# Kernel optimization log

Hardware: AMD Instinct MI355X
Metric: run time of the kernel (lower is better)

Reference implementation:

```python
import jax, jax.numpy as jnp
import numpy as np

B = 4096
HIST = 50
VOCAB = 100000
PAD_IDX = 179
EMB_DIM = 64           # sparse_dim_after_embedding
DENSE = 256            # dense_feature_number
PROJ_IN = 768          # emb_feature_dim_before_project
PROJ_HID = 256
PROJ_OUT = 64          # emb_feature_dim
BOT = (512, 64)        # bottom_mlp_dims
ALL_DIM = EMB_DIM + BOT[1] + PROJ_OUT        # 192
OUT_DIM = ALL_DIM * (ALL_DIM + 1) // 2 + BOT[1]  # 18592
TOP = (1024, 512)      # top_mlp_dims
BN_EPS = 1e-5

# precomputed upper-triangular (incl. diagonal) indices, row-major like torch mask extract
_TRIU_R, _TRIU_C = np.triu_indices(ALL_DIM)


def setup_inputs() -> dict:
    key = jax.random.key(0)
    ks = jax.random.split(key, 20)
    s = 0.02
    emb_table = jax.random.normal(ks[0], (VOCAB, EMB_DIM), jnp.float32) * s
    emb_table = emb_table.at[PAD_IDX].set(0.0)  # padding_idx=179
    return {
        "x_sparse": jax.random.randint(ks[1], (B, HIST), 0, VOCAB),
        "x_dense": jax.random.normal(ks[2], (B, DENSE), jnp.float32),
        "x_embed_before_projection": jax.random.normal(ks[3], (B, PROJ_IN), jnp.float32),
        "emb_table": emb_table,
        "pw1": jax.random.normal(ks[4], (PROJ_IN, PROJ_HID), jnp.float32) * s,
        "pb1": jnp.zeros((PROJ_HID,), jnp.float32),
        "pw2": jax.random.normal(ks[5], (PROJ_HID, PROJ_OUT), jnp.float32) * s,
        "pb2": jnp.zeros((PROJ_OUT,), jnp.float32),
        "bn_gamma": jnp.ones((PROJ_OUT,), jnp.float32),
        "bn_beta": jnp.zeros((PROJ_OUT,), jnp.float32),
        "bw1": jax.random.normal(ks[6], (DENSE, BOT[0]), jnp.float32) * s,
        "bb1": jnp.zeros((BOT[0],), jnp.float32),
        "bw2": jax.random.normal(ks[7], (BOT[0], BOT[1]), jnp.float32) * s,
        "bb2": jnp.zeros((BOT[1],), jnp.float32),
        "tw1": jax.random.normal(ks[8], (OUT_DIM, TOP[0]), jnp.float32) * s,
        "tb1": jnp.zeros((TOP[0],), jnp.float32),
        "tw2": jax.random.normal(ks[9], (TOP[0], TOP[1]), jnp.float32) * s,
        "tb2": jnp.zeros((TOP[1],), jnp.float32),
        "tw3": jax.random.normal(ks[10], (TOP[1], 1), jnp.float32) * s,
        "tb3": jnp.zeros((1,), jnp.float32),
    }


def reference(x_sparse, x_dense, x_embed_before_projection, emb_table,
              pw1, pb1, pw2, pb2, bn_gamma, bn_beta,
              bw1, bb1, bw2, bb2, tw1, tb1, tw2, tb2, tw3, tb3):
    # embedding-sum over history: [B, HIST, EMB_DIM] -> [B, EMB_DIM]
    embed_x = jnp.sum(emb_table[x_sparse], axis=1)

    # ContrastiveNet: Linear -> ReLU -> Linear -> BatchNorm1d (batch stats, training fwd)
    h = jax.nn.relu(x_embed_before_projection @ pw1 + pb1)
    z = h @ pw2 + pb2
    mu = jnp.mean(z, axis=0)
    var = jnp.var(z, axis=0)  # biased variance, as torch BN uses for normalization
    x_embed = bn_gamma * (z - mu) * jax.lax.rsqrt(var + BN_EPS) + bn_beta

    # bottom MLP (dropout = identity at inference)
    bottom = jax.nn.relu(jax.nn.relu(x_dense @ bw1 + bb1) @ bw2 + bb2)

    concat_first = jnp.concatenate([bottom, x_embed, embed_x], axis=-1)  # [B, 192]

    # pairwise dot-product interaction; pack upper triangle incl. diagonal
    dot = jnp.einsum('bi,bj->bij', concat_first, concat_first)  # [B, 192, 192]
    interaction = dot[:, _TRIU_R, _TRIU_C]  # [B, 192*193/2]

    concat_second = jnp.concatenate([interaction, bottom], axis=-1)  # [B, OUT_DIM]

    t = jax.nn.relu(concat_second @ tw1 + tb1)
    t = jax.nn.relu(t @ tw2 + tb2)
    output = jax.nn.sigmoid(t @ tw3 + tb3)  # [B, 1]
    # squeeze(-1).squeeze().unsqueeze(1) -> [B, 1]
    output = output.reshape(-1, 1)
    return output, x_embed
```

## Files before the change

### kernel.cpp

```cpp
#include <hip/hip_runtime.h>
#include <hip/hip_bf16.h>
#include <cstdint>
#include <cstddef>

typedef __bf16 bf16;
typedef unsigned char u8;
typedef unsigned short u16;
typedef __bf16 v8bf  __attribute__((ext_vector_type(8)));
typedef float  f32x4 __attribute__((ext_vector_type(4)));
typedef float  f32x16 __attribute__((ext_vector_type(16)));
typedef int    i32x4 __attribute__((ext_vector_type(4)));
typedef int    v8i32 __attribute__((ext_vector_type(8)));

__device__ __forceinline__ void async16(void* lds, const void* g) {
  __builtin_amdgcn_global_load_lds(
      (const __attribute__((address_space(1))) unsigned int*)g,
      (__attribute__((address_space(3))) unsigned int*)lds, 16, 0, 0);
}


__device__ __forceinline__ void pairs_dev(u16* __restrict__ pairs) {
  int r = threadIdx.x;
  if (r < 192) {
    int off = 192 * r - (r * (r - 1)) / 2;
    for (int c = r; c < 192; ++c) pairs[off + c - r] = (u16)((r << 8) | c);
  } else if (r == 192) {
    for (int j = 0; j < 64; ++j) pairs[18528 + j] = (u16)((j << 8) | 192);
  } else if (r == 193) {
    for (int j = 18592; j < 18624; ++j) pairs[j] = (u16)((192 << 8) | 192);
  }
}

__device__ __forceinline__ void packA_dev(const float* __restrict__ A,
                                          bf16* __restrict__ Ap, int K,
                                          int bx, int by) {
  const int t = threadIdx.x;
  const int KT = K >> 5;
  const size_t tile = ((size_t)bx * KT + by) * (64 * 32);
  const int c = t;
  const int mm = c >> 2, koct = (c & 3) * 8;
  const float* src = A + (size_t)(bx * 64 + mm) * K + by * 32 + koct;
  f32x4 f0 = *(const f32x4*)src;
  f32x4 f1 = *(const f32x4*)(src + 4);
  __align__(16) bf16 h[8];
  h[0]=(bf16)f0[0]; h[1]=(bf16)f0[1]; h[2]=(bf16)f0[2]; h[3]=(bf16)f0[3];
  h[4]=(bf16)f1[0]; h[5]=(bf16)f1[1]; h[6]=(bf16)f1[2]; h[7]=(bf16)f1[3];
  *(i32x4*)(Ap + tile + (size_t)c * 8) = *(const i32x4*)h;
}

__device__ __forceinline__ void packB_dev(const float* __restrict__ B,
                                          bf16* __restrict__ Bp, int K, int N,
                                          int bx, int by,
                                          float* __restrict__ sLB) {
  const int BNp = 64, LS = 66;
  const int t = threadIdx.x;
  const int KT = K >> 5;
  for (int idx = t; idx < 32 * BNp; idx += 256) {
    const int kk = idx >> 6, nn = idx & 63;
    sLB[kk * LS + nn] = B[(size_t)(by * 32 + kk) * N + bx * BNp + nn];
  }
  __syncthreads();
  const size_t tile = ((size_t)bx * KT + by) * ((size_t)BNp * 32);
  for (int c = t; c < BNp * 4; c += 256) {
    const int nn = c >> 2, koct = (c & 3) * 8;
    __align__(16) bf16 h[8];
#pragma unroll
    for (int j = 0; j < 8; ++j) h[j] = (bf16)sLB[(koct + j) * LS + nn];
    *(i32x4*)(Bp + tile + (size_t)c * 8) = *(const i32x4*)h;
  }
}

__device__ __forceinline__ void packTw1_dev(const float* __restrict__ tw1,
                                            u8* __restrict__ Bp, int nt, int kw,
                                            float* __restrict__ sLB) {
  const int t = threadIdx.x;
  u8* tile = Bp + ((size_t)nt * 291 + kw) * 8192;
#pragma unroll
  for (int ph = 0; ph < 2; ++ph) {
    if (ph) __syncthreads();
#pragma unroll
    for (int idx = t; idx < 1024; idx += 256) {
      const int kk = idx >> 5, nn4 = (idx & 31) * 4;
      const int gk = kw * 64 + ph * 32 + kk;
      f32x4 v = f32x4{0.f, 0.f, 0.f, 0.f};
      if (gk < 18592) {
        v = *(const f32x4*)(tw1 + (size_t)gk * 1024 + nt * 128 + nn4);
        v *= 32.f;
      }
      *(f32x4*)(sLB + kk * 132 + nn4) = v;
    }
    __syncthreads();
    const int nn = t >> 1;
    const int hkb = (t & 1) * 16;
    const int c = nn * 4 + ph * 2 + (t & 1);
    i32x4 d;
#pragma unroll
    for (int g = 0; g < 4; ++g) {
      const float p0 = sLB[(hkb + g * 4 + 0) * 132 + nn];
      const float p1 = sLB[(hkb + g * 4 + 1) * 132 + nn];
      const float p2 = sLB[(hkb + g * 4 + 2) * 132 + nn];
      const float p3 = sLB[(hkb + g * 4 + 3) * 132 + nn];
      int r = __builtin_amdgcn_cvt_pk_fp8_f32(p0, p1, 0, false);
      r = __builtin_amdgcn_cvt_pk_fp8_f32(p2, p3, r, true);
      d[g] = r;
    }
    *(i32x4*)(tile + c * 16) = d;
  }
}

__global__ __launch_bounds__(256) void prologue_kernel(
    const float* __restrict__ xep, const float* __restrict__ xd,
    const float* __restrict__ pw1, const float* __restrict__ pw2,
    const float* __restrict__ bw1, const float* __restrict__ bw2,
    const float* __restrict__ tw1, const float* __restrict__ tw2,
    bf16* Xp, bf16* Xd, bf16* Bpw1, bf16* Bpw2, bf16* Bbw1, bf16* Bbw2,
    u8* Btw1, bf16* Btw2, u16* pairs) {
  __shared__ float sLB[32 * 132];
  int i = blockIdx.x;
  if (i < 2328) { packTw1_dev(tw1, Btw1, i & 7, i >> 3, sLB); return; }
  i -= 2328;
  if (i < 1536) { packA_dev(xep, Xp, 768, i & 63, i >> 6); return; }
  i -= 1536;
  if (i < 512)  { packA_dev(xd, Xd, 256, i & 63, i >> 6); return; }
  i -= 512;
  if (i < 96)   { packB_dev(pw1, Bpw1, 768, 256, i & 3, i >> 2, sLB); return; }
  i -= 96;
  if (i < 8)    { packB_dev(pw2, Bpw2, 256, 64, 0, i, sLB); return; }
  i -= 8;
  if (i < 64)   { packB_dev(bw1, Bbw1, 256, 512, i & 7, i >> 3, sLB); return; }
  i -= 64;
  if (i < 16)   { packB_dev(bw2, Bbw2, 512, 64, 0, i, sLB); return; }
  i -= 16;
  if (i < 256)  { packB_dev(tw2, Btw2, 1024, 512, i & 7, i >> 3, sLB); return; }
  i -= 256;
  if (i == 0) pairs_dev(pairs);
}

__device__ __forceinline__ void embed8_dev(const int* __restrict__ xs,
                                           const float* __restrict__ emb,
                                           float* __restrict__ cf, int blk) {
  const int wid = threadIdx.x >> 6, lane = threadIdx.x & 63;
#pragma unroll
  for (int s = 0; s < 2; ++s) {
    const int b = blk * 8 + s * 4 + wid;
    const int* row = xs + (size_t)b * 50;
    float acc = 0.f;
#pragma unroll 10
    for (int h = 0; h < 50; ++h) {
      int idx = row[h];
      acc += emb[(size_t)idx * 64 + lane];
    }
    cf[(size_t)b * 193 + 128 + lane] = acc;
  }
}

template <int BM, int BN, int MF, int NF>
__device__ __forceinline__ void gemm_body(
    const bf16* __restrict__ Ap, const bf16* __restrict__ Bp,
    const float* __restrict__ bias,
    float* __restrict__ outF, int ldF,
    bf16* __restrict__ outP, int ktN, int bmsh,
    int KT, int M0, int relu_flag, int bx, int by,
    bf16* sA, bf16* sB) {
  const int t = threadIdx.x;
  const int wid = t >> 6, lane = t & 63;
  const int wm = (wid >> 1) * (MF * 16);
  const int wn = (wid & 1) * (NF * 16);
  const int r16 = lane & 15, q = lane >> 4;

  f32x4 acc[MF][NF];
#pragma unroll
  for (int i = 0; i < MF; ++i)
#pragma unroll
    for (int j = 0; j < NF; ++j) acc[i][j] = f32x4{0.f, 0.f, 0.f, 0.f};

  const bf16* aBase = Ap + (size_t)bx * KT * (BM * 32);
  const bf16* bBase = Bp + (size_t)by * KT * (BN * 32);
  constexpr int A_CH = BM * 4;
  constexpr int B_CH = BN * 4;

  for (int kt = 0; kt < KT; ++kt) {
    const bf16* ag = aBase + (size_t)kt * (BM * 32);
    const bf16* bg = bBase + (size_t)kt * (BN * 32);
#pragma unroll
    for (int c = t; c < A_CH; c += 256) {
      const int row = c >> 2, qs = c & 3, qg = (qs - (row >> 1)) & 3;
      async16(sA + c * 8, ag + row * 32 + qg * 8);
    }
#pragma unroll
    for (int c = t; c < B_CH; c += 256) {
      const int row = c >> 2, qs = c & 3, qg = (qs - (row >> 1)) & 3;
      async16(sB + c * 8, bg + row * 32 + qg * 8);
    }
    __syncthreads();
    v8bf af[MF], bfr[NF];
#pragma unroll
    for (int i = 0; i < MF; ++i) {
      const int row = wm + i * 16 + r16;
      af[i] = *(const v8bf*)(sA + row * 32 + (((q + (row >> 1)) & 3) * 8));
    }
#pragma unroll
    for (int j = 0; j < NF; ++j) {
      const int row = wn + j * 16 + r16;
      bfr[j] = *(const v8bf*)(sB + row * 32 + (((q + (row >> 1)) & 3) * 8));
    }
#pragma unroll
    for (int i = 0; i < MF; ++i)
#pragma unroll
      for (int j = 0; j < NF; ++j)
        acc[i][j] = __builtin_amdgcn_mfma_f32_16x16x32_bf16(af[i], bfr[j], acc[i][j], 0, 0, 0);
    __syncthreads();
  }

#pragma unroll
  for (int j = 0; j < NF; ++j) {
    const int gn = by * BN + wn + j * 16 + r16;
    const float bv = bias[gn];
#pragma unroll
    for (int i = 0; i < MF; ++i) {
      const int gm0 = M0 + bx * BM + wm + i * 16 + q * 4;
#pragma unroll
      for (int r = 0; r < 4; ++r) {
        float v = acc[i][j][r] + bv;
        if (relu_flag) v = fmaxf(v, 0.f);
        const int gm = gm0 + r;
        if (outF) outF[(size_t)gm * ldF + gn] = v;
        if (outP) {
          const int mt = gm >> bmsh, mm = gm & ((1 << bmsh) - 1);
          outP[(((size_t)mt * ktN + (gn >> 5)) << (bmsh + 5)) + ((size_t)mm << 5) + (gn & 31)] = (bf16)v;
        }
      }
    }
  }
}

template <int BM, int BN, int MF, int NF>
__global__ __launch_bounds__(256, 2) void gemm_kernel(
    const bf16* __restrict__ Ap, const bf16* __restrict__ Bp,
    const float* __restrict__ bias,
    float* __restrict__ outF, int ldF,
    bf16* __restrict__ outP, int ktN, int bmsh,
    int KT, int M0, int relu_flag) {
  __shared__ __align__(16) bf16 sA[BM * 32];
  __shared__ __align__(16) bf16 sB[BN * 32];
  gemm_body<BM, BN, MF, NF>(Ap, Bp, bias, outF, ldF, outP, ktN, bmsh,
                            KT, M0, relu_flag, blockIdx.x, blockIdx.y, sA, sB);
}

template <int BM, int BN, int MF, int NF>
__global__ __launch_bounds__(256, 2) void gemm_dual_kernel(
    const bf16* Ap0, const bf16* Bp0, const float* bias0,
    float* outF0, int ldF0, bf16* outP0, int ktN0, int bmsh0, int KT0, int relu0, int gy0,
    const bf16* Ap1, const bf16* Bp1, const float* bias1,
    float* outF1, int ldF1, bf16* outP1, int ktN1, int bmsh1, int KT1, int relu1, int gy1,
    const int* xs, const float* emb, float* cf) {
  __shared__ __align__(16) bf16 sA[BM * 32];
  __shared__ __align__(16) bf16 sB[BN * 32];
  if (blockIdx.z == 0) {
    if ((int)blockIdx.y >= gy0) return;
    gemm_body<BM, BN, MF, NF>(Ap0, Bp0, bias0, outF0, ldF0, outP0, ktN0, bmsh0,
                              KT0, 0, relu0, blockIdx.x, blockIdx.y, sA, sB);
  } else if (blockIdx.z == 1) {
    if ((int)blockIdx.y >= gy1) return;
    gemm_body<BM, BN, MF, NF>(Ap1, Bp1, bias1, outF1, ldF1, outP1, ktN1, bmsh1,
                              KT1, 0, relu1, blockIdx.x, blockIdx.y, sA, sB);
  } else {
    embed8_dev(xs, emb, cf, blockIdx.y * 64 + blockIdx.x);
  }
}

template <int S>
__global__ __launch_bounds__(256, 4) void gemm_splitk_mx(
    const u8* __restrict__ Ap, const u8* __restrict__ Bp,
    bf16* __restrict__ part, int Mchunk) {
  __shared__ __align__(16) u8 sAB[4][8192];
  const int t = threadIdx.x;
  const int bx = blockIdx.x, by = blockIdx.y, bz = blockIdx.z;
  const int lane = t & 63, wid = t >> 6;
  const int wm = (wid >> 1) * 64, wn = (wid & 1) * 64;
  const int l31 = lane & 31, khalf = lane >> 5;
  const int kw0 = (291 * bz) / S, kw1 = (291 * (bz + 1)) / S;

  const int r1 = t >> 2;
  const int g1 = r1 * 64 + ((((t & 3) - (r1 >> 1)) & 3) << 4);
  const int r2 = (t + 256) >> 2;
  const int g2 = r2 * 64 + (((((t + 256) & 3) - (r2 >> 1)) & 3) << 4);
  u8* lA = &sAB[0][0] + t * 16;
  u8* lB = &sAB[2][0] + t * 16;

  const u8* fa0[2]; const u8* fa1[2]; const u8* fb0[2]; const u8* fb1[2];
#pragma unroll
  for (int i = 0; i < 2; ++i) {
    const int ra = wm + i * 32 + l31;
    const int qa = (khalf * 2 + (ra >> 1)) & 3;
    fa0[i] = &sAB[0][0] + ra * 64 + qa * 16;
    fa1[i] = &sAB[0][0] + ra * 64 + (((qa + 1) & 3) << 4);
    const int rb = wn + i * 32 + l31;
    const int qb = (khalf * 2 + (rb >> 1)) & 3;
    fb0[i] = &sAB[2][0] + rb * 64 + qb * 16;
    fb1[i] = &sAB[2][0] + rb * 64 + (((qb + 1) & 3) << 4);
  }

  f32x16 acc[2][2];
#pragma unroll
  for (int i = 0; i < 2; ++i)
#pragma unroll
    for (int j = 0; j < 2; ++j)
#pragma unroll
      for (int r = 0; r < 16; ++r) acc[i][j][r] = 0.f;

  const u8* agp = Ap + ((size_t)bx * 291 + kw0) * 8192;
  const u8* bgp = Bp + ((size_t)by * 291 + kw0) * 8192;

  auto compute = [&](int off) {
    v8i32 av[2], bv[2];
#pragma unroll
    for (int i = 0; i < 2; ++i) {
      union { i32x4 h[2]; v8i32 v; } ua;
      ua.h[0] = *(const i32x4*)(fa0[i] + off);
      ua.h[1] = *(const i32x4*)(fa1[i] + off);
      av[i] = ua.v;
      union { i32x4 h[2]; v8i32 v; } ub;
      ub.h[0] = *(const i32x4*)(fb0[i] + off);
      ub.h[1] = *(const i32x4*)(fb1[i] + off);
      bv[i] = ub.v;
    }
#pragma unroll
    for (int i = 0; i < 2; ++i)
#pragma unroll
      for (int j = 0; j < 2; ++j)
        acc[i][j] = __builtin_amdgcn_mfma_scale_f32_32x32x64_f8f6f4(
            av[i], bv[j], acc[i][j], 0, 0,
            0, 0x7F7F7F7F,
            0, 0x7A7A7A7A);
  };

  const int nw = kw1 - kw0;
  int w = 0;
  for (; w + 2 <= nw; w += 2) {
    async16(lA, agp + g1);         async16(lA + 4096, agp + g2);
    async16(lB, bgp + g1);         async16(lB + 4096, bgp + g2);
    async16(lA + 8192, agp + 8192 + g1); async16(lA + 12288, agp + 8192 + g2);
    async16(lB + 8192, bgp + 8192 + g1); async16(lB + 12288, bgp + 8192 + g2);
    agp += 16384; bgp += 16384;
    __syncthreads();
    compute(0);
    compute(8192);
    __syncthreads();
  }
  if (w < nw) {
    async16(lA, agp + g1); async16(lA + 4096, agp + g2);
    async16(lB, bgp + g1); async16(lB + 4096, bgp + g2);
    __syncthreads();
    compute(0);
    __syncthreads();
  }

  bf16* pBase = part + (size_t)bz * Mchunk * 1024;
#pragma unroll
  for (int i = 0; i < 2; ++i)
#pragma unroll
    for (int j = 0; j < 2; ++j) {
      const int gn = by * 128 + wn + j * 32 + l31;
#pragma unroll
      for (int r = 0; r < 16; ++r) {
        const int gm = bx * 128 + wm + i * 32 + (r & 3) + 8 * (r >> 2) + 4 * khalf;
        pBase[(size_t)gm * 1024 + gn] = (bf16)acc[i][j][r];
      }
    }
}

__global__ __launch_bounds__(256) void reducek_kernel(const bf16* __restrict__ part,
                                                      const float* __restrict__ bias,
                                                      bf16* __restrict__ t1,
                                                      int S, int Mchunk, int M0) {
  const int idx = blockIdx.x * 256 + threadIdx.x;
  const int gm = idx >> 7;
  const int gn8 = (idx & 127) * 8;
  float v[8] = {0.f, 0.f, 0.f, 0.f, 0.f, 0.f, 0.f, 0.f};
  for (int s = 0; s < S; ++s) {
    v8bf p = *(const v8bf*)(part + ((size_t)s * Mchunk + gm) * 1024 + gn8);
#pragma unroll
    for (int r = 0; r < 8; ++r) v[r] += (float)p[r];
  }
  const f32x4 b0 = *(const f32x4*)(bias + gn8);
  const f32x4 b1 = *(const f32x4*)(bias + gn8 + 4);
  __align__(16) bf16 h[8];
#pragma unroll
  for (int r = 0; r < 4; ++r) h[r] = (bf16)fmaxf(v[r] + b0[r], 0.f);
#pragma unroll
  for (int r = 0; r < 4; ++r) h[4 + r] = (bf16)fmaxf(v[4 + r] + b1[r], 0.f);
  const int G = M0 + gm;
  const int mt = G >> 6, mm = G & 63, kt = gn8 >> 5;
  *(i32x4*)(t1 + (((size_t)mt * 32 + kt) << 11) + (mm << 5) + (gn8 & 31)) = *(const i32x4*)h;
}

__global__ __launch_bounds__(256) void bnstats_kernel(const float* __restrict__ z,
                                                      float* __restrict__ stats) {
  const int j = blockIdx.x, t = threadIdx.x;
  float s = 0.f, s2 = 0.f;
  for (int b = t; b < 4096; b += 256) {
    float v = z[(size_t)b * 64 + j];
    s += v; s2 += v * v;
  }
  __shared__ float sh[256], sh2[256];
  sh[t] = s; sh2[t] = s2;
  __syncthreads();
  for (int o = 128; o > 0; o >>= 1) {
    if (t < o) { sh[t] += sh[t + o]; sh2[t] += sh2[t + o]; }
    __syncthreads();
  }
  if (t == 0) {
    float mu = sh[0] * (1.f / 4096.f);
    float var = sh2[0] * (1.f / 4096.f) - mu * mu;
    stats[j] = mu;
    stats[64 + j] = rsqrtf(var + 1e-5f);
  }
}

__global__ __launch_bounds__(256, 2) void agen_kernel(const float* __restrict__ cf,
                                                      const float* __restrict__ z,
                                                      const float* __restrict__ stats,
                                                      const float* __restrict__ gamma,
                                                      const float* __restrict__ beta,
                                                      const u16* __restrict__ pairs,
                                                      u8* __restrict__ Ap,
                                                      float* __restrict__ dout,
                                                      int rowBase) {
  __shared__ float sCF[64 * 193];
  const int t = threadIdx.x;
  const int gRow0 = rowBase + blockIdx.x * 64;
  for (int idx = t; idx < 64 * 64; idx += 256) {
    const int r = idx >> 6, c = idx & 63;
    sCF[r * 193 + c] = cf[(size_t)(gRow0 + r) * 193 + c];
  }
  for (int idx = t; idx < 64 * 64; idx += 256) {
    const int r = idx >> 6, c = idx & 63;
    sCF[r * 193 + 128 + c] = cf[(size_t)(gRow0 + r) * 193 + 128 + c];
  }
  for (int idx = t; idx < 64 * 64; idx += 256) {
    const int r = idx >> 6, c = idx & 63;
    const float xe = gamma[c] * (z[(size_t)(gRow0 + r) * 64 + c] - stats[c]) * stats[64 + c] + beta[c];
    sCF[r * 193 + 64 + c] = xe;
    if (blockIdx.y == 0) dout[4096 + (size_t)(gRow0 + r) * 64 + c] = xe;
  }
  if (t < 64) sCF[t * 193 + 192] = 1.f;
  __syncthreads();

  const int kw0 = (291 * blockIdx.y) / 8;
  const int kw1 = (291 * (blockIdx.y + 1)) / 8;
  const int row = t >> 2, kq = t & 3;
  const int mt = blockIdx.x >> 1;
  const int mrow = (blockIdx.x & 1) * 64 + row;
  const float* myrow = sCF + row * 193;
  for (int kw = kw0; kw < kw1; ++kw) {
    const int kb = kw * 64 + kq * 16;
    i32x4 d;
    if (kb >= 18592) {
      d = i32x4{0, 0, 0, 0};
    } else {
      union { i32x4 v4[2]; u16 u[16]; } P;
      P.v4[0] = *(const i32x4*)(pairs + kb);
      P.v4[1] = *(const i32x4*)(pairs + kb + 8);
#pragma unroll
      for (int g = 0; g < 4; ++g) {
        float p[4];
#pragma unroll
        for (int j = 0; j < 4; ++j) {
          const u16 pr = P.u[g * 4 + j];
          p[j] = myrow[pr >> 8] * myrow[pr & 255];
        }
        int r = __builtin_amdgcn_cvt_pk_fp8_f32(p[0], p[1], 0, false);
        r = __builtin_amdgcn_cvt_pk_fp8_f32(p[2], p[3], r, true);
        d[g] = r;
      }
    }
    *(i32x4*)(Ap + (((size_t)mt * 291 + kw) * 128 + mrow) * 64 + kq * 16) = d;
  }
}

__global__ __launch_bounds__(256) void topdot_kernel(const float* __restrict__ t2,
                                                     const float* __restrict__ w,
                                                     const float* __restrict__ b3,
                                                     float* __restrict__ dout) {
  const int wid = threadIdx.x >> 6, lane = threadIdx.x & 63;
  const int b = blockIdx.x * 4 + wid;
  const f32x4* row = (const f32x4*)(t2 + (size_t)b * 512);
  const f32x4* wv = (const f32x4*)w;
  float s = 0.f;
#pragma unroll
  for (int i = 0; i < 2; ++i) {
    f32x4 a = row[lane * 2 + i], c = wv[lane * 2 + i];
    s += a[0] * c[0] + a[1] * c[1] + a[2] * c[2] + a[3] * c[3];
  }
  for (int m = 32; m > 0; m >>= 1) s += __shfl_xor(s, m, 64);
  if (lane == 0) dout[b] = 1.f / (1.f + __expf(-(s + b3[0])));
}

extern "C" void kernel_launch(void* const* d_in, const int* in_sizes, int n_in,
                              void* d_out, int out_size, void* d_ws, size_t ws_size,
                              hipStream_t stream) {
  const int*   xs   = (const int*)  d_in[0];
  const float* xd   = (const float*)d_in[1];
  const float* xep  = (const float*)d_in[2];
  const float* emb  = (const float*)d_in[3];
  const float* pw1  = (const float*)d_in[4];
  const float* pb1  = (const float*)d_in[5];
  const float* pw2  = (const float*)d_in[6];
  const float* pb2  = (const float*)d_in[7];
  const float* gmma = (const float*)d_in[8];
  const float* beta = (const float*)d_in[9];
  const float* bw1  = (const float*)d_in[10];
  const float* bb1  = (const float*)d_in[11];
  const float* bw2  = (const float*)d_in[12];
  const float* bb2  = (const float*)d_in[13];
  const float* tw1  = (const float*)d_in[14];
  const float* tb1  = (const float*)d_in[15];
  const float* tw2  = (const float*)d_in[16];
  const float* tb2  = (const float*)d_in[17];
  const float* tw3  = (const float*)d_in[18];
  const float* tb3  = (const float*)d_in[19];
  float* out = (float*)d_out;

  uint8_t* base = (uint8_t*)d_ws;
  size_t off = 0;
  auto alloc = [&](size_t b) {
    void* p = base + off;
    off = (off + b + 511) & ~((size_t)511);
    return p;
  };
  u16*  pairs = (u16*) alloc((size_t)18624 * 2);
  bf16* Xp    = (bf16*)alloc((size_t)4096 * 768 * 2);
  bf16* Xd    = (bf16*)alloc((size_t)4096 * 256 * 2);
  bf16* Bpw1  = (bf16*)alloc((size_t)768 * 256 * 2);
  bf16* Bpw2  = (bf16*)alloc((size_t)256 * 64 * 2);
  bf16* Bbw1  = (bf16*)alloc((size_t)256 * 512 * 2);
  bf16* Bbw2  = (bf16*)alloc((size_t)512 * 64 * 2);
  u8*   Btw1  = (u8*)  alloc((size_t)8 * 291 * 8192);
  bf16* Btw2  = (bf16*)alloc((size_t)1024 * 512 * 2);
  bf16* hbuf  = (bf16*)alloc((size_t)4096 * 256 * 2);
  float* z    = (float*)alloc((size_t)4096 * 64 * 4);
  float* stats= (float*)alloc((size_t)128 * 4);
  bf16* b0    = (bf16*)alloc((size_t)4096 * 512 * 2);
  float* cf   = (float*)alloc((size_t)4096 * 193 * 4);
  bf16* t1    = (bf16*)alloc((size_t)4096 * 1024 * 2);
  float* t2   = (float*)alloc((size_t)4096 * 512 * 4);
  size_t fixedEnd = off;

  int chunk = 512, S = 8;
  {
    const int candC[5] = {4096, 2048, 2048, 1024, 512};
    const int candS[5] = {4, 8, 4, 8, 8};
    for (int i = 0; i < 5; ++i) {
      size_t need = fixedEnd + (size_t)candC[i] * 18624 + 1024 +
                    (size_t)candS[i] * candC[i] * 1024 * 2 + 1024;
      if (need <= ws_size) { chunk = candC[i]; S = candS[i]; break; }
    }
  }
  u8*   ApBig = (u8*)  alloc((size_t)chunk * 18624);
  bf16* partK = (bf16*)alloc((size_t)S * chunk * 1024 * 2);

  prologue_kernel<<<4817, 256, 0, stream>>>(
      xep, xd, pw1, pw2, bw1, bw2, tw1, tw2,
      Xp, Xd, Bpw1, Bpw2, Bbw1, Bbw2, Btw1, Btw2, pairs);

  gemm_dual_kernel<64, 64, 2, 2><<<dim3(64, 8, 3), 256, 0, stream>>>(
      Xp, Bpw1, pb1, nullptr, 0, hbuf, 8, 6, 24, 1, 4,
      Xd, Bbw1, bb1, nullptr, 0, b0, 16, 6, 8, 1, 8,
      xs, emb, cf);
  gemm_dual_kernel<64, 64, 2, 2><<<dim3(64, 1, 2), 256, 0, stream>>>(
      hbuf, Bpw2, pb2, z, 64, nullptr, 0, 0, 8, 0, 1,
      b0, Bbw2, bb2, cf, 193, nullptr, 0, 0, 16, 1, 1,
      nullptr, nullptr, nullptr);

  bnstats_kernel<<<64, 256, 0, stream>>>(z, stats);

  for (int c0 = 0; c0 < 4096; c0 += chunk) {
    agen_kernel<<<dim3(chunk / 64, 8), 256, 0, stream>>>(
        cf, z, stats, gmma, beta, pairs, ApBig, out, c0);
    if (S == 4)
      gemm_splitk_mx<4><<<dim3(chunk / 128, 8, 4), 256, 0, stream>>>(
          ApBig, Btw1, partK, chunk);
    else
      gemm_splitk_mx<8><<<dim3(chunk / 128, 8, 8), 256, 0, stream>>>(
          ApBig, Btw1, partK, chunk);
    reducek_kernel<<<chunk / 2, 256, 0, stream>>>(partK, tb1, t1, S, chunk, c0);
  }

  gemm_kernel<64, 64, 2, 2><<<dim3(64, 8), 256, 0, stream>>>(
      t1, Btw2, tb2, t2, 512, nullptr, 0, 0, 32, 0, 1);
  topdot_kernel<<<1024, 256, 0, stream>>>(t2, tw3, tb3, out);
}
```

Baseline: 353.6 us.

## Fuse BN stats into GEMM epilogue, simplify tw1 packing, store t2 as bf16

Removes the separate batch-norm statistics kernel by accumulating column sums and sums of squares with atomics in the z GEMM epilogue, with the stats buffer zeroed in the prologue. The tw1 FP8 packing now goes directly from registers to the packed tile instead of staging through shared memory with barriers. The tw2 GEMM writes its output as packed bf16 for the final dot kernel rather than fp32. Risks: the atomic summation order is nondeterministic, the E[x^2]-mu^2 variance is computed from partial sums, and t2 loses precision in bf16.

```diff
diff --git a/kernel.cpp b/kernel.cpp
--- a/kernel.cpp
+++ b/kernel.cpp
@@ -10,6 +10,7 @@
 typedef float  f32x4 __attribute__((ext_vector_type(4)));
 typedef float  f32x16 __attribute__((ext_vector_type(16)));
 typedef int    i32x4 __attribute__((ext_vector_type(4)));
+typedef int    i32x2 __attribute__((ext_vector_type(2)));
 typedef int    v8i32 __attribute__((ext_vector_type(8)));
 
 __device__ __forceinline__ void async16(void* lds, const void* g) {
@@ -19,8 +20,9 @@
 }
 
 
-__device__ __forceinline__ void pairs_dev(u16* __restrict__ pairs) {
+__device__ __forceinline__ void pairs_dev(u16* __restrict__ pairs, float* __restrict__ stats) {
   int r = threadIdx.x;
+  if (r < 128) stats[r] = 0.f;
   if (r < 192) {
     int off = 192 * r - (r * (r - 1)) / 2;
     for (int c = r; c < 192; ++c) pairs[off + c - r] = (u16)((r << 8) | c);
@@ -71,40 +73,31 @@
 }
 
 __device__ __forceinline__ void packTw1_dev(const float* __restrict__ tw1,
-                                            u8* __restrict__ Bp, int nt, int kw,
-                                            float* __restrict__ sLB) {
+                                            u8* __restrict__ Bp, int nt, int kw) {
   const int t = threadIdx.x;
+  const int n4 = t & 31, k8 = t >> 5;
+  const int kbase = kw * 64 + k8 * 8;
+  const int nbase = nt * 128 + n4 * 4;
+  f32x4 v[8];
+#pragma unroll
+  for (int j = 0; j < 8; ++j) {
+    const int gk = kbase + j;
+    if (gk < 18592) {
+      v[j] = *(const f32x4*)(tw1 + (size_t)gk * 1024 + nbase);
+      v[j] *= 32.f;
+    } else {
+      v[j] = f32x4{0.f, 0.f, 0.f, 0.f};
+    }
+  }
   u8* tile = Bp + ((size_t)nt * 291 + kw) * 8192;
 #pragma unroll
-  for (int ph = 0; ph < 2; ++ph) {
-    if (ph) __syncthreads();
-#pragma unroll
-    for (int idx = t; idx < 1024; idx += 256) {
-      const int kk = idx >> 5, nn4 = (idx & 31) * 4;
-      const int gk = kw * 64 + ph * 32 + kk;
-      f32x4 v = f32x4{0.f, 0.f, 0.f, 0.f};
-      if (gk < 18592) {
-        v = *(const f32x4*)(tw1 + (size_t)gk * 1024 + nt * 128 + nn4);
-        v *= 32.f;
-      }
-      *(f32x4*)(sLB + kk * 132 + nn4) = v;
-    }
-    __syncthreads();
-    const int nn = t >> 1;
-    const int hkb = (t & 1) * 16;
-    const int c = nn * 4 + ph * 2 + (t & 1);
-    i32x4 d;
-#pragma unroll
-    for (int g = 0; g < 4; ++g) {
-      const float p0 = sLB[(hkb + g * 4 + 0) * 132 + nn];
-      const float p1 = sLB[(hkb + g * 4 + 1) * 132 + nn];
-      const float p2 = sLB[(hkb + g * 4 + 2) * 132 + nn];
-      const float p3 = sLB[(hkb + g * 4 + 3) * 132 + nn];
-      int r = __builtin_amdgcn_cvt_pk_fp8_f32(p0, p1, 0, false);
-      r = __builtin_amdgcn_cvt_pk_fp8_f32(p2, p3, r, true);
-      d[g] = r;
-    }
-    *(i32x4*)(tile + c * 16) = d;
+  for (int c = 0; c < 4; ++c) {
+    int r0 = __builtin_amdgcn_cvt_pk_fp8_f32(v[0][c], v[1][c], 0, false);
+    r0 = __builtin_amdgcn_cvt_pk_fp8_f32(v[2][c], v[3][c], r0, true);
+    int r1 = __builtin_amdgcn_cvt_pk_fp8_f32(v[4][c], v[5][c], 0, false);
+    r1 = __builtin_amdgcn_cvt_pk_fp8_f32(v[6][c], v[7][c], r1, true);
+    i32x2 d; d[0] = r0; d[1] = r1;
+    *(i32x2*)(tile + (n4 * 4 + c) * 64 + k8 * 8) = d;
   }
 }
 
@@ -114,10 +107,10 @@
     const float* __restrict__ bw1, const float* __restrict__ bw2,
     const float* __restrict__ tw1, const float* __restrict__ tw2,
     bf16* Xp, bf16* Xd, bf16* Bpw1, bf16* Bpw2, bf16* Bbw1, bf16* Bbw2,
-    u8* Btw1, bf16* Btw2, u16* pairs) {
-  __shared__ float sLB[32 * 132];
+    u8* Btw1, bf16* Btw2, u16* pairs, float* stats) {
+  __shared__ float sLB[32 * 66];
   int i = blockIdx.x;
-  if (i < 2328) { packTw1_dev(tw1, Btw1, i & 7, i >> 3, sLB); return; }
+  if (i < 2328) { packTw1_dev(tw1, Btw1, i & 7, i >> 3); return; }
   i -= 2328;
   if (i < 1536) { packA_dev(xep, Xp, 768, i & 63, i >> 6); return; }
   i -= 1536;
@@ -133,7 +126,7 @@
   i -= 16;
   if (i < 256)  { packB_dev(tw2, Btw2, 1024, 512, i & 7, i >> 3, sLB); return; }
   i -= 256;
-  if (i == 0) pairs_dev(pairs);
+  if (i == 0) pairs_dev(pairs, stats);
 }
 
 __device__ __forceinline__ void embed8_dev(const int* __restrict__ xs,
@@ -161,7 +154,7 @@
     float* __restrict__ outF, int ldF,
     bf16* __restrict__ outP, int ktN, int bmsh,
     int KT, int M0, int relu_flag, int bx, int by,
-    bf16* sA, bf16* sB) {
+    bf16* sA, bf16* sB, float* statsAcc) {
   const int t = threadIdx.x;
   const int wid = t >> 6, lane = t & 63;
   const int wm = (wid >> 1) * (MF * 16);
@@ -212,6 +205,10 @@
     __syncthreads();
   }
 
+  float cs[NF], cs2[NF];
+#pragma unroll
+  for (int j = 0; j < NF; ++j) { cs[j] = 0.f; cs2[j] = 0.f; }
+
 #pragma unroll
   for (int j = 0; j < NF; ++j) {
     const int gn = by * BN + wn + j * 16 + r16;
@@ -223,12 +220,27 @@
       for (int r = 0; r < 4; ++r) {
         float v = acc[i][j][r] + bv;
         if (relu_flag) v = fmaxf(v, 0.f);
+        if (statsAcc) { cs[j] += v; cs2[j] += v * v; }
         const int gm = gm0 + r;
         if (outF) outF[(size_t)gm * ldF + gn] = v;
         if (outP) {
           const int mt = gm >> bmsh, mm = gm & ((1 << bmsh) - 1);
           outP[(((size_t)mt * ktN + (gn >> 5)) << (bmsh + 5)) + ((size_t)mm << 5) + (gn & 31)] = (bf16)v;
         }
+      }
+    }
+  }
+
+  if (statsAcc) {
+#pragma unroll
+    for (int j = 0; j < NF; ++j) {
+      float a = cs[j], b2 = cs2[j];
+      a += __shfl_xor(a, 16, 64);  a += __shfl_xor(a, 32, 64);
+      b2 += __shfl_xor(b2, 16, 64); b2 += __shfl_xor(b2, 32, 64);
+      if (q == 0) {
+        const int gn = by * BN + wn + j * 16 + r16;
+        atomicAdd(&statsAcc[gn], a);
+        atomicAdd(&statsAcc[64 + gn], b2);
       }
     }
   }
@@ -244,13 +256,14 @@
   __shared__ __align__(16) bf16 sA[BM * 32];
   __shared__ __align__(16) bf16 sB[BN * 32];
   gemm_body<BM, BN, MF, NF>(Ap, Bp, bias, outF, ldF, outP, ktN, bmsh,
-                            KT, M0, relu_flag, blockIdx.x, blockIdx.y, sA, sB);
+                            KT, M0, relu_flag, blockIdx.x, blockIdx.y, sA, sB, nullptr);
 }
 
 template <int BM, int BN, int MF, int NF>
 __global__ __launch_bounds__(256, 2) void gemm_dual_kernel(
     const bf16* Ap0, const bf16* Bp0, const float* bias0,
     float* outF0, int ldF0, bf16* outP0, int ktN0, int bmsh0, int KT0, int relu0, int gy0,
+    float* statsAcc0,
     const bf16* Ap1, const bf16* Bp1, const float* bias1,
     float* outF1, int ldF1, bf16* outP1, int ktN1, int bmsh1, int KT1, int relu1, int gy1,
     const int* xs, const float* emb, float* cf) {
@@ -259,11 +272,11 @@
   if (blockIdx.z == 0) {
     if ((int)blockIdx.y >= gy0) return;
     gemm_body<BM, BN, MF, NF>(Ap0, Bp0, bias0, outF0, ldF0, outP0, ktN0, bmsh0,
-                              KT0, 0, relu0, blockIdx.x, blockIdx.y, sA, sB);
+                              KT0, 0, relu0, blockIdx.x, blockIdx.y, sA, sB, statsAcc0);
   } else if (blockIdx.z == 1) {
     if ((int)blockIdx.y >= gy1) return;
     gemm_body<BM, BN, MF, NF>(Ap1, Bp1, bias1, outF1, ldF1, outP1, ktN1, bmsh1,
-                              KT1, 0, relu1, blockIdx.x, blockIdx.y, sA, sB);
+                              KT1, 0, relu1, blockIdx.x, blockIdx.y, sA, sB, nullptr);
   } else {
     embed8_dev(xs, emb, cf, blockIdx.y * 64 + blockIdx.x);
   }
@@ -395,32 +408,9 @@
   *(i32x4*)(t1 + (((size_t)mt * 32 + kt) << 11) + (mm << 5) + (gn8 & 31)) = *(const i32x4*)h;
 }
 
-__global__ __launch_bounds__(256) void bnstats_kernel(const float* __restrict__ z,
-                                                      float* __restrict__ stats) {
-  const int j = blockIdx.x, t = threadIdx.x;
-  float s = 0.f, s2 = 0.f;
-  for (int b = t; b < 4096; b += 256) {
-    float v = z[(size_t)b * 64 + j];
-    s += v; s2 += v * v;
-  }
-  __shared__ float sh[256], sh2[256];
-  sh[t] = s; sh2[t] = s2;
-  __syncthreads();
-  for (int o = 128; o > 0; o >>= 1) {
-    if (t < o) { sh[t] += sh[t + o]; sh2[t] += sh2[t + o]; }
-    __syncthreads();
-  }
-  if (t == 0) {
-    float mu = sh[0] * (1.f / 4096.f);
-    float var = sh2[0] * (1.f / 4096.f) - mu * mu;
-    stats[j] = mu;
-    stats[64 + j] = rsqrtf(var + 1e-5f);
-  }
-}
-
 __global__ __launch_bounds__(256, 2) void agen_kernel(const float* __restrict__ cf,
                                                       const float* __restrict__ z,
-                                                      const float* __restrict__ stats,
+                                                      const float* __restrict__ gsum,
                                                       const float* __restrict__ gamma,
                                                       const float* __restrict__ beta,
                                                       const u16* __restrict__ pairs,
@@ -428,6 +418,7 @@
                                                       float* __restrict__ dout,
                                                       int rowBase) {
   __shared__ float sCF[64 * 193];
+  __shared__ float sMu[64], sRstd[64];
   const int t = threadIdx.x;
   const int gRow0 = rowBase + blockIdx.x * 64;
   for (int idx = t; idx < 64 * 64; idx += 256) {
@@ -438,13 +429,20 @@
     const int r = idx >> 6, c = idx & 63;
     sCF[r * 193 + 128 + c] = cf[(size_t)(gRow0 + r) * 193 + 128 + c];
   }
+  if (t < 64) {
+    const float mu = gsum[t] * (1.f / 4096.f);
+    const float var = gsum[64 + t] * (1.f / 4096.f) - mu * mu;
+    sMu[t] = mu;
+    sRstd[t] = rsqrtf(var + 1e-5f);
+    sCF[t * 193 + 192] = 1.f;
+  }
+  __syncthreads();
   for (int idx = t; idx < 64 * 64; idx += 256) {
     const int r = idx >> 6, c = idx & 63;
-    const float xe = gamma[c] * (z[(size_t)(gRow0 + r) * 64 + c] - stats[c]) * stats[64 + c] + beta[c];
+    const float xe = gamma[c] * (z[(size_t)(gRow0 + r) * 64 + c] - sMu[c]) * sRstd[c] + beta[c];
     sCF[r * 193 + 64 + c] = xe;
     if (blockIdx.y == 0) dout[4096 + (size_t)(gRow0 + r) * 64 + c] = xe;
   }
-  if (t < 64) sCF[t * 193 + 192] = 1.f;
   __syncthreads();
 
   const int kw0 = (291 * blockIdx.y) / 8;
@@ -479,20 +477,19 @@
   }
 }
 
-__global__ __launch_bounds__(256) void topdot_kernel(const float* __restrict__ t2,
+__global__ __launch_bounds__(256) void topdot_kernel(const bf16* __restrict__ t2p,
                                                      const float* __restrict__ w,
                                                      const float* __restrict__ b3,
                                                      float* __restrict__ dout) {
   const int wid = threadIdx.x >> 6, lane = threadIdx.x & 63;
   const int b = blockIdx.x * 4 + wid;
-  const f32x4* row = (const f32x4*)(t2 + (size_t)b * 512);
-  const f32x4* wv = (const f32x4*)w;
+  const size_t addr = ((((size_t)(b >> 6) * 16) + (lane >> 2)) << 11) +
+                      ((size_t)(b & 63) << 5) + (lane & 3) * 8;
+  v8bf p = *(const v8bf*)(t2p + addr);
+  const float* wv = w + lane * 8;
   float s = 0.f;
 #pragma unroll
-  for (int i = 0; i < 2; ++i) {
-    f32x4 a = row[lane * 2 + i], c = wv[lane * 2 + i];
-    s += a[0] * c[0] + a[1] * c[1] + a[2] * c[2] + a[3] * c[3];
-  }
+  for (int r = 0; r < 8; ++r) s += (float)p[r] * wv[r];
   for (int m = 32; m > 0; m >>= 1) s += __shfl_xor(s, m, 64);
   if (lane == 0) dout[b] = 1.f / (1.f + __expf(-(s + b3[0])));
 }
@@ -544,7 +541,7 @@
   bf16* b0    = (bf16*)alloc((size_t)4096 * 512 * 2);
   float* cf   = (float*)alloc((size_t)4096 * 193 * 4);
   bf16* t1    = (bf16*)alloc((size_t)4096 * 1024 * 2);
-  float* t2   = (float*)alloc((size_t)4096 * 512 * 4);
+  bf16* t2p   = (bf16*)alloc((size_t)4096 * 512 * 2);
   size_t fixedEnd = off;
 
   int chunk = 512, S = 8;
@@ -562,18 +559,16 @@
 
   prologue_kernel<<<4817, 256, 0, stream>>>(
       xep, xd, pw1, pw2, bw1, bw2, tw1, tw2,
-      Xp, Xd, Bpw1, Bpw2, Bbw1, Bbw2, Btw1, Btw2, pairs);
+      Xp, Xd, Bpw1, Bpw2, Bbw1, Bbw2, Btw1, Btw2, pairs, stats);
 
   gemm_dual_kernel<64, 64, 2, 2><<<dim3(64, 8, 3), 256, 0, stream>>>(
-      Xp, Bpw1, pb1, nullptr, 0, hbuf, 8, 6, 24, 1, 4,
+      Xp, Bpw1, pb1, nullptr, 0, hbuf, 8, 6, 24, 1, 4, nullptr,
       Xd, Bbw1, bb1, nullptr, 0, b0, 16, 6, 8, 1, 8,
       xs, emb, cf);
   gemm_dual_kernel<64, 64, 2, 2><<<dim3(64, 1, 2), 256, 0, stream>>>(
-      hbuf, Bpw2, pb2, z, 64, nullptr, 0, 0, 8, 0, 1,
+      hbuf, Bpw2, pb2, z, 64, nullptr, 0, 0, 8, 0, 1, stats,
       b0, Bbw2, bb2, cf, 193, nullptr, 0, 0, 16, 1, 1,
       nullptr, nullptr, nullptr);
-
-  bnstats_kernel<<<64, 256, 0, stream>>>(z, stats);
 
   for (int c0 = 0; c0 < 4096; c0 += chunk) {
     agen_kernel<<<dim3(chunk / 64, 8), 256, 0, stream>>>(
@@ -588,6 +583,6 @@
   }
 
   gemm_kernel<64, 64, 2, 2><<<dim3(64, 8), 256, 0, stream>>>(
-      t1, Btw2, tb2, t2, 512, nullptr, 0, 0, 32, 0, 1);
-  topdot_kernel<<<1024, 256, 0, stream>>>(t2, tw3, tb3, out);
-}
+      t1, Btw2, tb2, nullptr, 0, t2p, 16, 6, 32, 0, 1);
+  topdot_kernel<<<1024, 256, 0, stream>>>(t2p, tw3, tb3, out);
+}
```

Measured after the change: 341.9 us. -3.3%, faster.
